# Optimization experiments

Hardware: AMD Instinct MI355X
Metric: run time of the kernel (lower is better)

The kernel has to match this reference:

```python
import jax, jax.numpy as jnp
import numpy as np

B, P, N, E, H, D = 8, 1000, 1000, 128, 8, 16  # batch, pomo, nodes, embed, heads, qkv_dim
SQRT_E = float(np.sqrt(E))
CLIP = 10.0
INV_SQRT_D = 1.0 / float(np.sqrt(D))


def _heads(x):
    # [b, n, H*D] -> [b, H, n, D]
    b, n, _ = x.shape
    return x.reshape(b, n, H, D).transpose(0, 2, 1, 3)


def _mha(q, k, v, ninf_mask):
    # q: [b,H,P,D], k/v: [b,H,N,D], ninf_mask: [b,P,N]
    score = jnp.einsum('bhnd,bhsd->bhns', q, k) * INV_SQRT_D
    score = score + ninf_mask[:, None, :, :]
    w = jax.nn.softmax(score, axis=-1)
    out = jnp.einsum('bhns,bhsd->bhnd', w, v)
    return out.transpose(0, 2, 1, 3).reshape(q.shape[0], q.shape[2], H * D)


def setup_inputs() -> dict:
    key = jax.random.key(0)
    ks = jax.random.split(key, 16)
    s = 0.02
    return {
        'encoded_last_node': jax.random.normal(ks[0], (B, P, E), jnp.float32),
        'attr': jax.random.normal(ks[1], (B, P, 4), jnp.float32),
        'encoded_nodes': jax.random.normal(ks[2], (B, N, E), jnp.float32),
        'ninf_mask': jnp.zeros((B, P, N), jnp.float32),
        'Wq_shared': jax.random.normal(ks[3], (E + 4, H * D), jnp.float32) * s,
        'Wk_shared': jax.random.normal(ks[4], (E, H * D), jnp.float32) * s,
        'Wv_shared': jax.random.normal(ks[5], (E, H * D), jnp.float32) * s,
        'Wq_task': jax.random.normal(ks[6], (E + 4, H * D), jnp.float32) * s,
        'Wk_task': jax.random.normal(ks[7], (E, H * D), jnp.float32) * s,
        'Wv_task': jax.random.normal(ks[8], (E, H * D), jnp.float32) * s,
        'Wc_shared': jax.random.normal(ks[9], (H * D, E), jnp.float32) * s,
        'bc_shared': jnp.zeros((E,), jnp.float32),
        'Wc_task': jax.random.normal(ks[10], (H * D, E), jnp.float32) * s,
        'bc_task': jnp.zeros((E,), jnp.float32),
        'Wg': jax.random.normal(ks[11], (E + 4, E), jnp.float32) * s,
        'bg': jnp.zeros((E,), jnp.float32),
    }


def reference(encoded_last_node, attr, encoded_nodes, ninf_mask,
              Wq_shared, Wk_shared, Wv_shared, Wq_task, Wk_task, Wv_task,
              Wc_shared, bc_shared, Wc_task, bc_task, Wg, bg):
    # set_kv
    k_shared = _heads(encoded_nodes @ Wk_shared)
    v_shared = _heads(encoded_nodes @ Wv_shared)
    k_task = _heads(encoded_nodes @ Wk_task)
    v_task = _heads(encoded_nodes @ Wv_task)

    # decoder forward
    input_cat = jnp.concatenate([encoded_last_node, attr], axis=2)  # [B,P,E+4]
    q_shared = _heads(input_cat @ Wq_shared)
    q_task = _heads(input_cat @ Wq_task)

    out_shared = _mha(q_shared, k_shared, v_shared, ninf_mask) @ Wc_shared + bc_shared
    out_task = _mha(q_task, k_task, v_task, ninf_mask) @ Wc_task + bc_task

    gate = jax.nn.sigmoid(input_cat @ Wg + bg)
    gated_out = gate * out_shared + (1.0 - gate) * out_task  # [B,P,E]

    # pointer scores against single-head key (encoded_nodes)
    score = jnp.einsum('bpe,bne->bpn', gated_out, encoded_nodes) / SQRT_E
    score_clipped = CLIP * jnp.tanh(score)
    probs = jax.nn.softmax(score_clipped + ninf_mask, axis=2)
    return probs
```

## Files before the change

### kernel.cpp

```cpp
#include <hip/hip_runtime.h>
#include <math.h>

#define BB 8
#define PP 1000
#define NN 1000
#define EE 128
#define HH 8
#define DD 16

#define INV_SQRT_E 0.08838834764831845f
#define INV_SQRT_D 0.25f

typedef short short8_t __attribute__((ext_vector_type(8)));
typedef float f32x4    __attribute__((ext_vector_type(4)));
typedef __bf16 bf16x4  __attribute__((ext_vector_type(4)));
typedef __bf16 bf16x8  __attribute__((ext_vector_type(8)));

__device__ __forceinline__ float sigmoid_fast(float x) {
    return 1.f / (1.f + __expf(-x));
}
__device__ __forceinline__ float tanh_fast(float x) {
    x = fminf(fmaxf(x, -15.f), 15.f);
    float e = __expf(2.f * x);
    return (e - 1.f) / (e + 1.f);
}

__device__ __forceinline__ f32x4 mfma16(short8_t a, short8_t b, f32x4 c) {
    return __builtin_amdgcn_mfma_f32_16x16x32_bf16(a, b, c, 0, 0, 0);
}

__device__ __forceinline__ float sum16(float x) {
    int v;
    v = __builtin_amdgcn_update_dpp(0, __builtin_bit_cast(int, x), 0xB1, 0xF, 0xF, true);
    x += __builtin_bit_cast(float, v);
    v = __builtin_amdgcn_update_dpp(0, __builtin_bit_cast(int, x), 0x4E, 0xF, 0xF, true);
    x += __builtin_bit_cast(float, v);
    v = __builtin_amdgcn_update_dpp(0, __builtin_bit_cast(int, x), 0x141, 0xF, 0xF, true);
    x += __builtin_bit_cast(float, v);
    v = __builtin_amdgcn_update_dpp(0, __builtin_bit_cast(int, x), 0x140, 0xF, 0xF, true);
    x += __builtin_bit_cast(float, v);
    return x;
}

__device__ __forceinline__ unsigned int pack_bf16(float a, float b) {
    __bf16 x = (__bf16)a, y = (__bf16)b;
    unsigned short ux = __builtin_bit_cast(unsigned short, x);
    unsigned short uy = __builtin_bit_cast(unsigned short, y);
    return (unsigned int)ux | ((unsigned int)uy << 16);
}

__global__ __launch_bounds__(256) void conv_w_kernel(
    const float* __restrict__ Wk_s, const float* __restrict__ Wv_s,
    const float* __restrict__ Wk_t, const float* __restrict__ Wv_t,
    const float* __restrict__ Wq_s, const float* __restrict__ Wq_t,
    const float* __restrict__ Wg,   const float* __restrict__ Wc_s,
    const float* __restrict__ Wc_t, __bf16* __restrict__ Wtb)
{
    const int m = blockIdx.x, kt = blockIdx.y;
    const float* srcs[9] = {Wk_s, Wv_s, Wk_t, Wv_t, Wq_s, Wq_t, Wg, Wc_s, Wc_t};
    const int   srcKs[9] = {128, 128, 128, 128, 132, 132, 132, 128, 128};
    const int   kpads[9] = {128, 128, 128, 128, 160, 160, 160, 128, 128};
    const size_t offs[9] = {0, 16384, 32768, 49152, 65536, 86016, 106496, 126976, 143360};
    const int kp = kpads[m];
    if (kt * 32 >= kp) return;
    const float* src = srcs[m];
    const int sK = srcKs[m];
    const size_t off = offs[m];
    __shared__ float tile[32][129];
    const int tid = threadIdx.x;
    for (int j = tid; j < 32 * 128; j += 256) {
        int kk = j >> 7, n = j & 127;
        int k = kt * 32 + kk;
        tile[kk][n] = (k < sK) ? src[(size_t)k * 128 + n] : 0.f;
    }
    __syncthreads();
    for (int j = tid; j < 32 * 128; j += 256) {
        int n = j >> 5, kk = j & 31;
        Wtb[off + (size_t)n * kp + kt * 32 + kk] = (__bf16)tile[kk][n];
    }
}

__global__ __launch_bounds__(256) void to_bf16_kernel(
    const float* __restrict__ in, __bf16* __restrict__ outb)
{
    int i = (blockIdx.x * 256 + threadIdx.x) * 4;
    float4 v = *(const float4*)&in[i];
    bf16x4 pk = { (__bf16)v.x, (__bf16)v.y, (__bf16)v.z, (__bf16)v.w };
    *(bf16x4*)&outb[i] = pk;
}

__global__ __launch_bounds__(256) void concat_inb_kernel(
    const float* __restrict__ eln, const float* __restrict__ attr,
    __bf16* __restrict__ inb)
{
    int t = blockIdx.x * 256 + threadIdx.x;
    int row = t / 20, seg = t - row * 20;
    bf16x8 o = {};
    if (seg < 16) {
        const float* p = &eln[(size_t)row * 128 + seg * 8];
        float4 a = *(const float4*)p, b = *(const float4*)(p + 4);
        o = bf16x8{ (__bf16)a.x, (__bf16)a.y, (__bf16)a.z, (__bf16)a.w,
                    (__bf16)b.x, (__bf16)b.y, (__bf16)b.z, (__bf16)b.w };
    } else if (seg == 16) {
        float4 a = *(const float4*)&attr[(size_t)row * 4];
        o = bf16x8{ (__bf16)a.x, (__bf16)a.y, (__bf16)a.z, (__bf16)a.w,
                    (__bf16)0.f, (__bf16)0.f, (__bf16)0.f, (__bf16)0.f };
    }
    *(bf16x8*)&inb[(size_t)row * 160 + seg * 8] = o;
}

template<int NC>
__device__ __forceinline__ void proj_body(
    const __bf16* __restrict__ A, const __bf16* __restrict__ W,
    f32x4 acc[8], int r0, int quad, int lq)
{
    const int K = NC * 32;
    short8_t aF[NC];
    #pragma unroll
    for (int c = 0; c < NC; ++c)
        aF[c] = *(const short8_t*)&A[(size_t)(r0 + lq) * K + c * 32 + quad * 8];
    #pragma unroll
    for (int nt = 0; nt < 8; ++nt) {
        acc[nt] = f32x4{0.f, 0.f, 0.f, 0.f};
        #pragma unroll
        for (int c = 0; c < NC; ++c) {
            short8_t bF = *(const short8_t*)&W[(size_t)(nt * 16 + lq) * K + c * 32 + quad * 8];
            acc[nt] = mfma16(aF[c], bF, acc[nt]);
        }
    }
}

__global__ __launch_bounds__(256) void proj_mfma_kernel(
    const __bf16* __restrict__ nodesb, const __bf16* __restrict__ inb,
    const __bf16* __restrict__ Wtb, const float* __restrict__ bg,
    __bf16* __restrict__ kb_s, __bf16* __restrict__ vt_s,
    __bf16* __restrict__ kb_t, __bf16* __restrict__ vt_t,
    __bf16* __restrict__ qb_s, __bf16* __restrict__ qb_t,
    float* __restrict__ gate)
{
    const int wsel = blockIdx.y;
    const int wave = threadIdx.x >> 6, lane = threadIdx.x & 63;
    const int quad = lane >> 4, lq = lane & 15;
    const int r0 = blockIdx.x * 64 + wave * 16;

    f32x4 acc[8];
    if (wsel < 4) {
        proj_body<4>(nodesb, Wtb + (size_t)wsel * 16384, acc, r0, quad, lq);
    } else {
        proj_body<5>(inb, Wtb + 65536 + (size_t)(wsel - 4) * 20480, acc, r0, quad, lq);
    }

    if (wsel == 0 || wsel == 2 || wsel == 4 || wsel == 5) {
        __bf16* O = (wsel == 0) ? kb_s : (wsel == 2) ? kb_t : (wsel == 4) ? qb_s : qb_t;
        #pragma unroll
        for (int r = 0; r < 4; ++r) {
            int m = r0 + quad * 4 + r;
            int b = m / 1000, n = m - b * 1000;
            #pragma unroll
            for (int nt = 0; nt < 8; ++nt)
                O[(((size_t)(b * 8 + nt) * 1000 + n) << 4) + lq] = (__bf16)acc[nt][r];
        }
    } else if (wsel == 1 || wsel == 3) {
        __bf16* O = (wsel == 1) ? vt_s : vt_t;
        #pragma unroll
        for (int r = 0; r < 4; ++r) {
            int m = r0 + quad * 4 + r;
            int b = m / 1000, n = m - b * 1000;
            int rr = n & 31;
            int pos = (n & ~31) + ((rr < 16) ? (rr << 1) : (((rr - 16) << 1) | 1));
            #pragma unroll
            for (int nt = 0; nt < 8; ++nt)
                O[(((size_t)(b * 8 + nt) * 16 + lq) << 10) + pos] = (__bf16)acc[nt][r];
        }
    } else {
        #pragma unroll
        for (int nt = 0; nt < 8; ++nt) {
            float bias = bg[nt * 16 + lq];
            #pragma unroll
            for (int r = 0; r < 4; ++r) {
                int m = r0 + quad * 4 + r;
                gate[(size_t)m * 128 + nt * 16 + lq] = sigmoid_fast(acc[nt][r] + bias);
            }
        }
    }
}

__global__ __launch_bounds__(256) void attn_mfma_kernel(
    const __bf16* __restrict__ qb_s, const __bf16* __restrict__ qb_t,
    const __bf16* __restrict__ kb_s, const __bf16* __restrict__ kb_t,
    const __bf16* __restrict__ vt_s, const __bf16* __restrict__ vt_t,
    const float* __restrict__ mask,
    float* __restrict__ att_s, float* __restrict__ att_t)
{
    const int b    = blockIdx.z;
    const int wave = threadIdx.x >> 6;
    const int combo = blockIdx.y * 4 + wave;
    const int br = combo & 1;
    const int h  = combo >> 1;
    const __bf16* Q  = br ? qb_t : qb_s;
    const __bf16* K  = br ? kb_t : kb_s;
    const __bf16* Vt = br ? vt_t : vt_s;
    float* O         = br ? att_t : att_s;
    const int lane = threadIdx.x & 63;
    const int quad = lane >> 4, lq = lane & 15;
    const int bh = b * HH + h;
    const int p0 = blockIdx.x * 32;

    __shared__ unsigned int Plds[4][2][16][20];

    short8_t qA[2] = {};
    if (quad < 2) {
        #pragma unroll
        for (int t = 0; t < 2; ++t) {
            int p = p0 + t * 16 + lq; if (p > 999) p = 999;
            qA[t] = *(const short8_t*)&Q[(((size_t)bh * 1000 + p) << 4) + quad * 8];
        }
    }
    short8_t onesB = { (short)0x3F80, (short)0x3F80, (short)0x3F80, (short)0x3F80,
                       (short)0x3F80, (short)0x3F80, (short)0x3F80, (short)0x3F80 };

    f32x4 o[2] = { {0.f,0.f,0.f,0.f}, {0.f,0.f,0.f,0.f} };
    f32x4 l[2] = { {0.f,0.f,0.f,0.f}, {0.f,0.f,0.f,0.f} };

    const float* mbase[2][4];
    #pragma unroll
    for (int t = 0; t < 2; ++t)
        #pragma unroll
        for (int r = 0; r < 4; ++r) {
            int p = p0 + t * 16 + quad * 4 + r; if (p > 999) p = 999;
            mbase[t][r] = mask + ((size_t)b * 1000 + p) * 1000;
        }

    short8_t kB0c = {}, kB1c = {};
    if (quad < 2) {
        kB0c = *(const short8_t*)&K[(((size_t)bh * 1000 + lq) << 4) + quad * 8];
        kB1c = *(const short8_t*)&K[(((size_t)bh * 1000 + 16 + lq) << 4) + quad * 8];
    }
    short8_t vBc = *(const short8_t*)&Vt[(((size_t)bh * 16 + lq) << 10) + quad * 8];
    float mkc[2][8];
    #pragma unroll
    for (int t = 0; t < 2; ++t)
        #pragma unroll
        for (int r = 0; r < 4; ++r) {
            mkc[t][r]     = mbase[t][r][lq];
            mkc[t][4 + r] = mbase[t][r][16 + lq];
        }

    for (int n0 = 0; n0 < 992; n0 += 32) {
        int c0 = n0 + 32 + lq;      if (c0 > 999) c0 = 999;
        int c1 = n0 + 48 + lq;      if (c1 > 999) c1 = 999;
        short8_t kB0n = {}, kB1n = {};
        if (quad < 2) {
            kB0n = *(const short8_t*)&K[(((size_t)bh * 1000 + c0) << 4) + quad * 8];
            kB1n = *(const short8_t*)&K[(((size_t)bh * 1000 + c1) << 4) + quad * 8];
        }
        short8_t vBn = *(const short8_t*)&Vt[(((size_t)bh * 16 + lq) << 10) + n0 + 32 + quad * 8];
        float mkn[2][8];
        #pragma unroll
        for (int t = 0; t < 2; ++t)
            #pragma unroll
            for (int r = 0; r < 4; ++r) {
                mkn[t][r]     = mbase[t][r][c0];
                mkn[t][4 + r] = mbase[t][r][c1];
            }

        #pragma unroll
        for (int t = 0; t < 2; ++t) {
            f32x4 zero = {0.f, 0.f, 0.f, 0.f};
            f32x4 s0 = mfma16(qA[t], kB0c, zero);
            f32x4 s1 = mfma16(qA[t], kB1c, zero);
            float e0[4], e1[4];
            #pragma unroll
            for (int r = 0; r < 4; ++r) {
                e0[r] = __expf(fmaf(s0[r], INV_SQRT_D, mkc[t][r]));
                e1[r] = __expf(fmaf(s1[r], INV_SQRT_D, mkc[t][4 + r]));
            }
            __threadfence_block();
            #pragma unroll
            for (int r = 0; r < 4; ++r)
                Plds[wave][t][quad * 4 + r][lq] = pack_bf16(e0[r], e1[r]);
            __threadfence_block();
            uint4 u4 = *(const uint4*)&Plds[wave][t][lq][quad * 4];
            short8_t aP = __builtin_bit_cast(short8_t, u4);
            o[t] = mfma16(aP, vBc, o[t]);
            l[t] = mfma16(aP, onesB, l[t]);
        }

        kB0c = kB0n; kB1c = kB1n; vBc = vBn;
        #pragma unroll
        for (int t = 0; t < 2; ++t)
            #pragma unroll
            for (int j = 0; j < 8; ++j) mkc[t][j] = mkn[t][j];
    }

    #pragma unroll
    for (int t = 0; t < 2; ++t) {
        f32x4 zero = {0.f, 0.f, 0.f, 0.f};
        f32x4 s0 = mfma16(qA[t], kB0c, zero);
        float e0[4];
        #pragma unroll
        for (int r = 0; r < 4; ++r)
            e0[r] = (lq < 8) ? __expf(fmaf(s0[r], INV_SQRT_D, mkc[t][r])) : 0.f;
        __threadfence_block();
        #pragma unroll
        for (int r = 0; r < 4; ++r)
            Plds[wave][t][quad * 4 + r][lq] = pack_bf16(e0[r], 0.f);
        __threadfence_block();
        uint4 u4 = *(const uint4*)&Plds[wave][t][lq][quad * 4];
        short8_t aP = __builtin_bit_cast(short8_t, u4);
        o[t] = mfma16(aP, vBc, o[t]);
        l[t] = mfma16(aP, onesB, l[t]);
    }

    #pragma unroll
    for (int t = 0; t < 2; ++t)
        #pragma unroll
        for (int r = 0; r < 4; ++r) {
            int p = p0 + t * 16 + quad * 4 + r;
            if (p < 1000)
                O[((size_t)b * 1000 + p) * 128 + h * 16 + lq] = o[t][r] / l[t][r];
        }
}

__global__ __launch_bounds__(256) void combine_mfma_kernel(
    const float* __restrict__ att_s, const float* __restrict__ att_t,
    const __bf16* __restrict__ Wtb,
    const float* __restrict__ bc_s, const float* __restrict__ bc_t,
    const float* __restrict__ gate, __bf16* __restrict__ gatedb)
{
    const int wave = threadIdx.x >> 6, lane = threadIdx.x & 63;
    const int quad = lane >> 4, lq = lane & 15;
    const int r0 = blockIdx.x * 64 + wave * 16;
    const __bf16* Ws = Wtb + 126976;
    const __bf16* Wt = Wtb + 143360;

    short8_t aS[4], aT[4];
    #pragma unroll
    for (int c = 0; c < 4; ++c) {
        const float* ps = &att_s[(size_t)(r0 + lq) * 128 + c * 32 + quad * 8];
        const float* pt = &att_t[(size_t)(r0 + lq) * 128 + c * 32 + quad * 8];
        float4 x = *(const float4*)ps, y = *(const float4*)(ps + 4);
        bf16x8 s8 = { (__bf16)x.x, (__bf16)x.y, (__bf16)x.z, (__bf16)x.w,
                      (__bf16)y.x, (__bf16)y.y, (__bf16)y.z, (__bf16)y.w };
        aS[c] = __builtin_bit_cast(short8_t, s8);
        x = *(const float4*)pt; y = *(const float4*)(pt + 4);
        bf16x8 t8 = { (__bf16)x.x, (__bf16)x.y, (__bf16)x.z, (__bf16)x.w,
                      (__bf16)y.x, (__bf16)y.y, (__bf16)y.z, (__bf16)y.w };
        aT[c] = __builtin_bit_cast(short8_t, t8);
    }
    f32x4 accS[8], accT[8];
    #pragma unroll
    for (int nt = 0; nt < 8; ++nt) {
        accS[nt] = f32x4{0.f,0.f,0.f,0.f};
        accT[nt] = f32x4{0.f,0.f,0.f,0.f};
        #pragma unroll
        for (int c = 0; c < 4; ++c) {
            short8_t bS = *(const short8_t*)&Ws[(size_t)(nt * 16 + lq) * 128 + c * 32 + quad * 8];
            short8_t bT = *(const short8_t*)&Wt[(size_t)(nt * 16 + lq) * 128 + c * 32 + quad * 8];
            accS[nt] = mfma16(aS[c], bS, accS[nt]);
            accT[nt] = mfma16(aT[c], bT, accT[nt]);
        }
    }
    #pragma unroll
    for (int nt = 0; nt < 8; ++nt) {
        int f = nt * 16 + lq;
        float b1 = bc_s[f], b2 = bc_t[f];
        #pragma unroll
        for (int r = 0; r < 4; ++r) {
            int m = r0 + quad * 4 + r;
            float g = gate[(size_t)m * 128 + f];
            float val = g * (accS[nt][r] + b1) + (1.f - g) * (accT[nt][r] + b2);
            gatedb[(size_t)m * 128 + f] = (__bf16)val;
        }
    }
}

__global__ __launch_bounds__(256) void pointer_softmax_kernel(
    const __bf16* __restrict__ gb, const __bf16* __restrict__ nb,
    const float* __restrict__ mask, float* __restrict__ out)
{
    const int b    = blockIdx.y;
    const int p0   = blockIdx.x * 16;
    const int wave = threadIdx.x >> 6;
    const int lane = threadIdx.x & 63;
    const int quad = lane >> 4, lq = lane & 15;

    __shared__ float Spart[4][16];

    short8_t aF[4];
    {
        int pp = p0 + lq; if (pp > 999) pp = 999;
        const __bf16* arow = gb + (((size_t)b * 1000 + pp) << 7) + quad * 8;
        #pragma unroll
        for (int kc = 0; kc < 4; ++kc) aF[kc] = *(const short8_t*)&arow[kc * 32];
    }

    float ev[16][4];
    float psum[4] = {0.f, 0.f, 0.f, 0.f};

    #pragma unroll
    for (int i = 0; i < 16; ++i) {
        const int nt = i * 4 + wave;
        const int nn = nt * 16 + lq;
        const bool nv = nn < 1000;
        int nc = nv ? nn : 999;
        const __bf16* brow = nb + (((size_t)b * 1000 + nc) << 7) + quad * 8;
        f32x4 acc = {0.f, 0.f, 0.f, 0.f};
        #pragma unroll
        for (int kc = 0; kc < 4; ++kc) {
            short8_t bF = *(const short8_t*)&brow[kc * 32];
            acc = mfma16(aF[kc], bF, acc);
        }
        #pragma unroll
        for (int r = 0; r < 4; ++r) {
            int p = p0 + quad * 4 + r;
            bool v = nv && (p < 1000);
            size_t midx = v ? ((size_t)b * 1000 + p) * 1000 + nn : 0;
            float mk = mask[midx];
            float sc = 10.f * tanh_fast(acc[r] * INV_SQRT_E);
            float ee = v ? __expf(sc + mk) : 0.f;
            ev[i][r] = ee;
            psum[r] += ee;
        }
    }

    #pragma unroll
    for (int r = 0; r < 4; ++r) psum[r] = sum16(psum[r]);
    if (lq == 0) {
        #pragma unroll
        for (int r = 0; r < 4; ++r) Spart[wave][quad * 4 + r] = psum[r];
    }
    __syncthreads();
    float inv[4];
    #pragma unroll
    for (int r = 0; r < 4; ++r) {
        int row = quad * 4 + r;
        float s = Spart[0][row] + Spart[1][row] + Spart[2][row] + Spart[3][row];
        inv[r] = 1.f / s;
    }

    #pragma unroll
    for (int i = 0; i < 16; ++i) {
        const int nt = i * 4 + wave;
        const int nn = nt * 16 + lq;
        if (nn < 1000) {
            #pragma unroll
            for (int r = 0; r < 4; ++r) {
                int p = p0 + quad * 4 + r;
                if (p < 1000)
                    out[((size_t)b * 1000 + p) * 1000 + nn] = ev[i][r] * inv[r];
            }
        }
    }
}

extern "C" void kernel_launch(void* const* d_in, const int* in_sizes, int n_in,
                              void* d_out, int out_size, void* d_ws, size_t ws_size,
                              hipStream_t stream)
{
    const float* eln   = (const float*)d_in[0];
    const float* attr  = (const float*)d_in[1];
    const float* nodes = (const float*)d_in[2];
    const float* mask  = (const float*)d_in[3];
    const float* Wq_s  = (const float*)d_in[4];
    const float* Wk_s  = (const float*)d_in[5];
    const float* Wv_s  = (const float*)d_in[6];
    const float* Wq_t  = (const float*)d_in[7];
    const float* Wk_t  = (const float*)d_in[8];
    const float* Wv_t  = (const float*)d_in[9];
    const float* Wc_s  = (const float*)d_in[10];
    const float* bc_s  = (const float*)d_in[11];
    const float* Wc_t  = (const float*)d_in[12];
    const float* bc_t  = (const float*)d_in[13];
    const float* Wg    = (const float*)d_in[14];
    const float* bg    = (const float*)d_in[15];
    float* out = (float*)d_out;

    char* w = (char*)d_ws;
    const size_t KB_SZ = (size_t)8 * 8 * 1000 * 16 * 2;
    const size_t VT_SZ = (size_t)8 * 8 * 16 * 1024 * 2;
    const size_t F_SZ  = (size_t)8000 * 128 * 4;
    const size_t H_SZ  = (size_t)8000 * 128 * 2;
    const size_t IN_SZ = (size_t)8000 * 160 * 2;
    __bf16* kb_s = (__bf16*)w;            w += KB_SZ;
    __bf16* kb_t = (__bf16*)w;            w += KB_SZ;
    __bf16* qb_s = (__bf16*)w;            w += KB_SZ;
    __bf16* qb_t = (__bf16*)w;            w += KB_SZ;
    __bf16* vt_s = (__bf16*)w;            w += VT_SZ;
    __bf16* vt_t = (__bf16*)w;            w += VT_SZ;
    float* gate  = (float*)w;             w += F_SZ;
    float* att_s = (float*)w;             w += F_SZ;
    float* att_t = (float*)w;             w += F_SZ;
    __bf16* gatedb = (__bf16*)w;          w += H_SZ;
    __bf16* nodesb = (__bf16*)w;          w += H_SZ;
    __bf16* inb    = (__bf16*)w;          w += IN_SZ;
    __bf16* Wtb    = (__bf16*)w;          w += 320000;

    hipMemsetAsync(vt_s, 0, 2 * VT_SZ, stream);

    conv_w_kernel<<<dim3(9, 5), 256, 0, stream>>>(
        Wk_s, Wv_s, Wk_t, Wv_t, Wq_s, Wq_t, Wg, Wc_s, Wc_t, Wtb);
    to_bf16_kernel<<<dim3(1000), 256, 0, stream>>>(nodes, nodesb);
    concat_inb_kernel<<<dim3(625), 256, 0, stream>>>(eln, attr, inb);
    proj_mfma_kernel<<<dim3(125, 7), 256, 0, stream>>>(
        nodesb, inb, Wtb, bg, kb_s, vt_s, kb_t, vt_t, qb_s, qb_t, gate);
    attn_mfma_kernel<<<dim3(32, 4, 8), 256, 0, stream>>>(
        qb_s, qb_t, kb_s, kb_t, vt_s, vt_t, mask, att_s, att_t);
    combine_mfma_kernel<<<dim3(125), 256, 0, stream>>>(
        att_s, att_t, Wtb, bc_s, bc_t, gate, gatedb);
    pointer_softmax_kernel<<<dim3(63, 8), 256, 0, stream>>>(
        gatedb, nodesb, mask, out);
}
```

Measured before the change: 250.0 us.

## Compute attention scores with one 32x32x16 MFMA per tile instead of four

```diff
diff --git a/kernel.cpp b/kernel.cpp
--- a/kernel.cpp
+++ b/kernel.cpp
@@ -13,6 +13,7 @@
 
 typedef short short8_t __attribute__((ext_vector_type(8)));
 typedef float f32x4    __attribute__((ext_vector_type(4)));
+typedef float f32x16   __attribute__((ext_vector_type(16)));
 typedef __bf16 bf16x4  __attribute__((ext_vector_type(4)));
 typedef __bf16 bf16x8  __attribute__((ext_vector_type(8)));
 
@@ -27,6 +28,9 @@
 
 __device__ __forceinline__ f32x4 mfma16(short8_t a, short8_t b, f32x4 c) {
     return __builtin_amdgcn_mfma_f32_16x16x32_bf16(a, b, c, 0, 0, 0);
+}
+__device__ __forceinline__ f32x16 mfma32(short8_t a, short8_t b, f32x16 c) {
+    return __builtin_amdgcn_mfma_f32_32x32x16_bf16(a, b, c, 0, 0, 0);
 }
 
 __device__ __forceinline__ float sum16(float x) {
@@ -203,113 +207,96 @@
     float* O         = br ? att_t : att_s;
     const int lane = threadIdx.x & 63;
     const int quad = lane >> 4, lq = lane & 15;
+    const int col  = lane & 31;
+    const int half = lane >> 5;
     const int bh = b * HH + h;
     const int p0 = blockIdx.x * 32;
 
-    __shared__ unsigned int Plds[4][2][16][20];
-
-    short8_t qA[2] = {};
-    if (quad < 2) {
-        #pragma unroll
-        for (int t = 0; t < 2; ++t) {
-            int p = p0 + t * 16 + lq; if (p > 999) p = 999;
-            qA[t] = *(const short8_t*)&Q[(((size_t)bh * 1000 + p) << 4) + quad * 8];
-        }
-    }
+    __shared__ __align__(16) __bf16 S[4][32][36];
+
+    int pq = p0 + col; if (pq > 999) pq = 999;
+    short8_t qA = *(const short8_t*)&Q[(((size_t)bh * 1000 + pq) << 4) + half * 8];
+
     short8_t onesB = { (short)0x3F80, (short)0x3F80, (short)0x3F80, (short)0x3F80,
                        (short)0x3F80, (short)0x3F80, (short)0x3F80, (short)0x3F80 };
 
     f32x4 o[2] = { {0.f,0.f,0.f,0.f}, {0.f,0.f,0.f,0.f} };
     f32x4 l[2] = { {0.f,0.f,0.f,0.f}, {0.f,0.f,0.f,0.f} };
 
-    const float* mbase[2][4];
-    #pragma unroll
-    for (int t = 0; t < 2; ++t)
-        #pragma unroll
-        for (int r = 0; r < 4; ++r) {
-            int p = p0 + t * 16 + quad * 4 + r; if (p > 999) p = 999;
-            mbase[t][r] = mask + ((size_t)b * 1000 + p) * 1000;
-        }
-
-    short8_t kB0c = {}, kB1c = {};
-    if (quad < 2) {
-        kB0c = *(const short8_t*)&K[(((size_t)bh * 1000 + lq) << 4) + quad * 8];
-        kB1c = *(const short8_t*)&K[(((size_t)bh * 1000 + 16 + lq) << 4) + quad * 8];
-    }
+    const float* mrow[8];
+    #pragma unroll
+    for (int j = 0; j < 8; ++j) {
+        int row = p0 + ((2 * j) & 3) + 8 * (j >> 1) + 4 * half;
+        if (row > 998) row = 998;
+        mrow[j] = mask + ((size_t)b * 1000 + row) * 1000 + col;
+    }
+
+    short8_t kBc = *(const short8_t*)&K[(((size_t)bh * 1000 + col) << 4) + half * 8];
     short8_t vBc = *(const short8_t*)&Vt[(((size_t)bh * 16 + lq) << 10) + quad * 8];
-    float mkc[2][8];
-    #pragma unroll
-    for (int t = 0; t < 2; ++t)
-        #pragma unroll
-        for (int r = 0; r < 4; ++r) {
-            mkc[t][r]     = mbase[t][r][lq];
-            mkc[t][4 + r] = mbase[t][r][16 + lq];
-        }
 
     for (int n0 = 0; n0 < 992; n0 += 32) {
-        int c0 = n0 + 32 + lq;      if (c0 > 999) c0 = 999;
-        int c1 = n0 + 48 + lq;      if (c1 > 999) c1 = 999;
-        short8_t kB0n = {}, kB1n = {};
-        if (quad < 2) {
-            kB0n = *(const short8_t*)&K[(((size_t)bh * 1000 + c0) << 4) + quad * 8];
-            kB1n = *(const short8_t*)&K[(((size_t)bh * 1000 + c1) << 4) + quad * 8];
-        }
+        int nk = n0 + 32 + col; if (nk > 999) nk = 999;
+        short8_t kBn = *(const short8_t*)&K[(((size_t)bh * 1000 + nk) << 4) + half * 8];
         short8_t vBn = *(const short8_t*)&Vt[(((size_t)bh * 16 + lq) << 10) + n0 + 32 + quad * 8];
-        float mkn[2][8];
-        #pragma unroll
-        for (int t = 0; t < 2; ++t)
-            #pragma unroll
-            for (int r = 0; r < 4; ++r) {
-                mkn[t][r]     = mbase[t][r][c0];
-                mkn[t][4 + r] = mbase[t][r][c1];
-            }
+
+        float mk[16];
+        #pragma unroll
+        for (int j = 0; j < 8; ++j) {
+            mk[2 * j]     = mrow[j][0];
+            mk[2 * j + 1] = mrow[j][1000];
+            mrow[j] += 32;
+        }
+
+        f32x16 s = mfma32(qA, kBc, f32x16{});
+
+        __threadfence_block();
+        #pragma unroll
+        for (int reg = 0; reg < 16; ++reg) {
+            float e = __expf(fmaf(s[reg], INV_SQRT_D, mk[reg]));
+            S[wave][(reg & 3) + 8 * (reg >> 2) + 4 * half][col] = (__bf16)e;
+        }
+        __threadfence_block();
 
         #pragma unroll
         for (int t = 0; t < 2; ++t) {
-            f32x4 zero = {0.f, 0.f, 0.f, 0.f};
-            f32x4 s0 = mfma16(qA[t], kB0c, zero);
-            f32x4 s1 = mfma16(qA[t], kB1c, zero);
-            float e0[4], e1[4];
-            #pragma unroll
-            for (int r = 0; r < 4; ++r) {
-                e0[r] = __expf(fmaf(s0[r], INV_SQRT_D, mkc[t][r]));
-                e1[r] = __expf(fmaf(s1[r], INV_SQRT_D, mkc[t][4 + r]));
-            }
-            __threadfence_block();
-            #pragma unroll
-            for (int r = 0; r < 4; ++r)
-                Plds[wave][t][quad * 4 + r][lq] = pack_bf16(e0[r], e1[r]);
-            __threadfence_block();
-            uint4 u4 = *(const uint4*)&Plds[wave][t][lq][quad * 4];
+            uint2 L = *(const uint2*)&S[wave][t * 16 + lq][quad * 4];
+            uint2 H = *(const uint2*)&S[wave][t * 16 + lq][16 + quad * 4];
+            unsigned u0 = __builtin_amdgcn_perm(H.x, L.x, 0x05040100u);
+            unsigned u1 = __builtin_amdgcn_perm(H.x, L.x, 0x07060302u);
+            unsigned u2 = __builtin_amdgcn_perm(H.y, L.y, 0x05040100u);
+            unsigned u3 = __builtin_amdgcn_perm(H.y, L.y, 0x07060302u);
+            uint4 u4 = make_uint4(u0, u1, u2, u3);
             short8_t aP = __builtin_bit_cast(short8_t, u4);
             o[t] = mfma16(aP, vBc, o[t]);
             l[t] = mfma16(aP, onesB, l[t]);
         }
-
-        kB0c = kB0n; kB1c = kB1n; vBc = vBn;
-        #pragma unroll
-        for (int t = 0; t < 2; ++t)
-            #pragma unroll
-            for (int j = 0; j < 8; ++j) mkc[t][j] = mkn[t][j];
-    }
-
-    #pragma unroll
-    for (int t = 0; t < 2; ++t) {
-        f32x4 zero = {0.f, 0.f, 0.f, 0.f};
-        f32x4 s0 = mfma16(qA[t], kB0c, zero);
-        float e0[4];
-        #pragma unroll
-        for (int r = 0; r < 4; ++r)
-            e0[r] = (lq < 8) ? __expf(fmaf(s0[r], INV_SQRT_D, mkc[t][r])) : 0.f;
+        kBc = kBn; vBc = vBn;
+    }
+
+    {
+        f32x16 s = mfma32(qA, kBc, f32x16{});
         __threadfence_block();
         #pragma unroll
-        for (int r = 0; r < 4; ++r)
-            Plds[wave][t][quad * 4 + r][lq] = pack_bf16(e0[r], 0.f);
+        for (int reg = 0; reg < 16; ++reg) {
+            int j = reg >> 1;
+            float mkv = (col < 8) ? ((reg & 1) ? mrow[j][1000] : mrow[j][0]) : 0.f;
+            float e = (col < 8) ? __expf(fmaf(s[reg], INV_SQRT_D, mkv)) : 0.f;
+            S[wave][(reg & 3) + 8 * (reg >> 2) + 4 * half][col] = (__bf16)e;
+        }
         __threadfence_block();
-        uint4 u4 = *(const uint4*)&Plds[wave][t][lq][quad * 4];
-        short8_t aP = __builtin_bit_cast(short8_t, u4);
-        o[t] = mfma16(aP, vBc, o[t]);
-        l[t] = mfma16(aP, onesB, l[t]);
+        #pragma unroll
+        for (int t = 0; t < 2; ++t) {
+            uint2 L = *(const uint2*)&S[wave][t * 16 + lq][quad * 4];
+            uint2 H = *(const uint2*)&S[wave][t * 16 + lq][16 + quad * 4];
+            unsigned u0 = __builtin_amdgcn_perm(H.x, L.x, 0x05040100u);
+            unsigned u1 = __builtin_amdgcn_perm(H.x, L.x, 0x07060302u);
+            unsigned u2 = __builtin_amdgcn_perm(H.y, L.y, 0x05040100u);
+            unsigned u3 = __builtin_amdgcn_perm(H.y, L.y, 0x07060302u);
+            uint4 u4 = make_uint4(u0, u1, u2, u3);
+            short8_t aP = __builtin_bit_cast(short8_t, u4);
+            o[t] = mfma16(aP, vBc, o[t]);
+            l[t] = mfma16(aP, onesB, l[t]);
+        }
     }
 
     #pragma unroll
```

Measured after the change: 242.1 us. 1.03x faster.
